# Optimization experiments

Hardware: AMD Instinct MI355X
Metric: run time of the kernel (lower is better)

The kernel has to match this reference:

```python
import jax, jax.numpy as jnp
import numpy as np

B, N, F, S, OUT = 8, 12000, 128, 16, 128

def setup_inputs() -> dict:
    key = jax.random.key(0)
    k1, k2, k3, k4 = jax.random.split(key, 4)
    x = jax.random.normal(k1, (B, N, F), dtype=jnp.float32)
    # Linear(in_c*spiral_size, out_c): weight [out, in], bias [out]
    bound = 1.0 / np.sqrt(F * S)
    W = jax.random.uniform(k2, (OUT, F * S), dtype=jnp.float32, minval=-bound, maxval=bound)
    b = jax.random.uniform(k3, (OUT,), dtype=jnp.float32, minval=-bound, maxval=bound)
    spiral_adj = jax.random.randint(k4, (1, N, S), 0, N, dtype=jnp.int32)
    zero_padding = jnp.ones((1, N, 1), dtype=jnp.float32)
    return {"x": x, "W": W, "b": b, "spiral_adj": spiral_adj, "zero_padding": zero_padding}

def reference(x, W, b, spiral_adj, zero_padding):
    # x: [B, N, F]; spiral_adj: [1, N, S] vertex indices shared across batch
    idx = spiral_adj[0]                         # [N, S]
    spirals = x[:, idx, :]                      # [B, N, S, F] gather along vertex dim
    bsz, npts, s, f = spirals.shape
    spirals = spirals.reshape(bsz, npts, s * f)  # [B, N, S*F]
    out = jnp.einsum('bnk,ok->bno', spirals, W) + b  # [B, N, OUT]
    out = jax.nn.relu(out)
    return out * zero_padding
```

## Files before the change

kernel.cpp:

```cpp
#include <hip/hip_runtime.h>

#define BATCH 8
#define NPTS  12000
#define FDIM  128
#define SDIM  16
#define ODIM  128
#define KDIM  (SDIM * FDIM)
#define MTOT  (BATCH * NPTS)

#define BM 128
#define BK 64

#define NTILES 94
#define XELEMS (BATCH * NPTS * FDIM)
#define WELEMS (ODIM * KDIM)
#define XBYTES ((size_t)XELEMS * 2)
#define WBYTES ((size_t)WELEMS * 2)

typedef __bf16 bf16x4 __attribute__((ext_vector_type(4)));
typedef __bf16 bf16x8 __attribute__((ext_vector_type(8)));
typedef float  f32x4  __attribute__((ext_vector_type(4)));
typedef float  f32x8  __attribute__((ext_vector_type(8)));

#define AS1(p) ((const __attribute__((address_space(1))) void*)(p))
#define AS3(p) ((__attribute__((address_space(3))) void*)(p))

#define CVT_XBLK 6000
#define CVT_WBLK 128
#define CVT_BPB  750

__global__ __launch_bounds__(256)
void cvt_f32_bf16(const float* __restrict__ x, const float* __restrict__ W,
                  __bf16* __restrict__ xb, __bf16* __restrict__ Wb) {
    const int blk = blockIdx.x;
    const float* __restrict__ src;
    __bf16* __restrict__ dst;
    size_t base;
    if (blk < CVT_XBLK) {
        const int b = blk & 7;
        const int c = blk >> 3;
        base = ((size_t)b * CVT_BPB + c) * (256 * 8) + (size_t)threadIdx.x * 8;
        src = x;  dst = xb;
    } else {
        base = (size_t)(blk - CVT_XBLK) * (256 * 8) + (size_t)threadIdx.x * 8;
        src = W;  dst = Wb;
    }
    const f32x8 v = *reinterpret_cast<const f32x8*>(src + base);
    bf16x8 h;
#pragma unroll
    for (int e = 0; e < 8; ++e) h[e] = (__bf16)v[e];
    *reinterpret_cast<bf16x8*>(dst + base) = h;
}

__global__ __launch_bounds__(256, 2)
void spiral_gemm_bf16(const __bf16* __restrict__ xb,
                      const __bf16* __restrict__ Wb,
                      const float*  __restrict__ bias,
                      const int*    __restrict__ idx,
                      const float*  __restrict__ zp,
                      float*        __restrict__ out)
{
    __shared__ __bf16 As[2][BM * BK];
    __shared__ __bf16 Ws[2][ODIM * BK];
    __shared__ int    idxS[BM * SDIM];

    const int tid   = threadIdx.x;
    const int wave  = tid >> 6;
    const int lane  = tid & 63;
    const int batch = blockIdx.x & 7;
    const int n0    = (blockIdx.x >> 3) * BM;

    const int lrow8 = lane >> 3;
    const int clog  = (lane & 7) ^ lrow8;

    const __bf16* xbase = xb + (size_t)batch * (NPTS * FDIM);

    {
        const int row  = tid >> 1, half = tid & 1;
        const int n    = n0 + row;
        const int nrow = n < NPTS ? n : NPTS - 1;
        const int4* s4 = reinterpret_cast<const int4*>(idx + nrow * SDIM + half * 8);
        int4* d4       = reinterpret_cast<int4*>(&idxS[row * SDIM + half * 8]);
        d4[0] = s4[0];
        d4[1] = s4[1];
    }
    __syncthreads();

    int rrow[4];
#pragma unroll
    for (int p = 0; p < 4; ++p) rrow[p] = (p * 4 + wave) * 8 + lrow8;

    int gCur[4], gNext[4];
#pragma unroll
    for (int p = 0; p < 4; ++p) gCur[p] = idxS[rrow[p] * SDIM + 0];

    auto issue = [&](int buf, int kt, const int* g) {
        const int f0 = (kt & 1) * BK;
#pragma unroll
        for (int p = 0; p < 4; ++p) {
            const int r0 = (p * 4 + wave) * 8;
            const __bf16* ga = xbase + (size_t)g[p] * FDIM + f0 + clog * 8;
            __builtin_amdgcn_global_load_lds(AS1(ga), AS3(&As[buf][r0 * BK]), 16, 0, 0);
            const __bf16* gw = Wb + (size_t)(r0 + lrow8) * KDIM + kt * BK + clog * 8;
            __builtin_amdgcn_global_load_lds(AS1(gw), AS3(&Ws[buf][r0 * BK]), 16, 0, 0);
        }
    };

    f32x4 acc[4][4];
#pragma unroll
    for (int i = 0; i < 4; ++i)
#pragma unroll
        for (int j = 0; j < 4; ++j)
            acc[i][j] = f32x4{0.f, 0.f, 0.f, 0.f};

    const int wm   = (wave >> 1) * 64;
    const int wn   = (wave & 1) * 64;
    const int lrow = lane & 15;
    const int quad = lane >> 4;

    auto compute = [&](int buf) {
#pragma unroll
        for (int kk = 0; kk < 2; ++kk) {
            const int ph = (kk * 4 + quad) ^ (lrow & 7);
            bf16x8 a[4], b[4];
#pragma unroll
            for (int i = 0; i < 4; ++i)
                a[i] = *reinterpret_cast<const bf16x8*>(
                    &As[buf][(wm + i * 16 + lrow) * BK + ph * 8]);
#pragma unroll
            for (int j = 0; j < 4; ++j)
                b[j] = *reinterpret_cast<const bf16x8*>(
                    &Ws[buf][(wn + j * 16 + lrow) * BK + ph * 8]);
#pragma unroll
            for (int i = 0; i < 4; ++i)
#pragma unroll
                for (int j = 0; j < 4; ++j)
                    acc[i][j] = __builtin_amdgcn_mfma_f32_16x16x32_bf16(
                        a[i], b[j], acc[i][j], 0, 0, 0);
        }
    };

    issue(0, 0, gCur);

    for (int t = 0; t < 16; ++t) {
        issue(1, 2 * t + 1, gCur);
        asm volatile("s_waitcnt vmcnt(8)" ::: "memory");
        asm volatile("s_barrier" ::: "memory");
        if (t < 15) {
#pragma unroll
            for (int p = 0; p < 4; ++p)
                gNext[p] = idxS[rrow[p] * SDIM + t + 1];
        }
        compute(0);
        asm volatile("s_barrier" ::: "memory");

        if (t < 15) {
            issue(0, 2 * t + 2, gNext);
            asm volatile("s_waitcnt vmcnt(8)" ::: "memory");
        } else {
            asm volatile("s_waitcnt vmcnt(0)" ::: "memory");
        }
        asm volatile("s_barrier" ::: "memory");
        compute(1);
        asm volatile("s_barrier" ::: "memory");
#pragma unroll
        for (int p = 0; p < 4; ++p) gCur[p] = gNext[p];
    }

#pragma unroll
    for (int i = 0; i < 4; ++i) {
#pragma unroll
        for (int r = 0; r < 4; ++r) {
            const int row = wm + i * 16 + quad * 4 + r;
            const int n   = n0 + row;
            if (n < NPTS) {
                const float z = zp[n];
                float* orow   = out + ((size_t)batch * NPTS + n) * ODIM;
#pragma unroll
                for (int j = 0; j < 4; ++j) {
                    const int col = wn + j * 16 + lrow;
                    float v = acc[i][j][r] + bias[col];
                    v = fmaxf(v, 0.f);
                    orow[col] = v * z;
                }
            }
        }
    }
}

#define LDA 72
__global__ __launch_bounds__(256, 2)
void spiral_gemm_fp32(const float* __restrict__ x, const float* __restrict__ W,
                      const float* __restrict__ bias, const int* __restrict__ idx,
                      const float* __restrict__ zp, float* __restrict__ out)
{
    __shared__ __bf16 Asf[BM * LDA];
    __shared__ __bf16 Wsf[ODIM * LDA];
    const int tid = threadIdx.x, wave = tid >> 6, lane = tid & 63;
    const int m0 = blockIdx.x * BM;
    const int srow = tid >> 3, schunk = tid & 7;
    int a_n[4]; const float* a_xb[4];
#pragma unroll
    for (int p = 0; p < 4; ++p) {
        int m = m0 + srow + p * 32, bb = m / NPTS;
        a_n[p] = m - bb * NPTS; a_xb[p] = x + (size_t)bb * (NPTS * FDIM);
    }
    f32x4 acc[4][4];
#pragma unroll
    for (int i = 0; i < 4; ++i)
#pragma unroll
        for (int j = 0; j < 4; ++j) acc[i][j] = f32x4{0.f,0.f,0.f,0.f};
    const int wm = (wave >> 1) * 64, wn = (wave & 1) * 64;
    const int lrow = lane & 15, quad = lane >> 4;
    for (int kt = 0; kt < KDIM / BK; ++kt) {
        const int s = kt >> 1, f0 = (kt & 1) * BK;
        __syncthreads();
#pragma unroll
        for (int p = 0; p < 4; ++p) {
            const int r = srow + p * 32;
            const int g = idx[a_n[p] * SDIM + s];
            const f32x8 v = *reinterpret_cast<const f32x8*>(
                a_xb[p] + (size_t)g * FDIM + f0 + schunk * 8);
            bf16x8 h;
#pragma unroll
            for (int e = 0; e < 8; ++e) h[e] = (__bf16)v[e];
            *reinterpret_cast<bf16x8*>(&Asf[r * LDA + schunk * 8]) = h;
            const f32x8 w = *reinterpret_cast<const f32x8*>(
                W + (size_t)r * KDIM + kt * BK + schunk * 8);
            bf16x8 hw;
#pragma unroll
            for (int e = 0; e < 8; ++e) hw[e] = (__bf16)w[e];
            *reinterpret_cast<bf16x8*>(&Wsf[r * LDA + schunk * 8]) = hw;
        }
        __syncthreads();
#pragma unroll
        for (int kk = 0; kk < 2; ++kk) {
            const int koff = kk * 32 + quad * 8;
            bf16x8 a[4], b[4];
#pragma unroll
            for (int i = 0; i < 4; ++i)
                a[i] = *reinterpret_cast<const bf16x8*>(&Asf[(wm + i*16 + lrow)*LDA + koff]);
#pragma unroll
            for (int j = 0; j < 4; ++j)
                b[j] = *reinterpret_cast<const bf16x8*>(&Wsf[(wn + j*16 + lrow)*LDA + koff]);
#pragma unroll
            for (int i = 0; i < 4; ++i)
#pragma unroll
                for (int j = 0; j < 4; ++j)
                    acc[i][j] = __builtin_amdgcn_mfma_f32_16x16x32_bf16(a[i], b[j], acc[i][j], 0,0,0);
        }
    }
#pragma unroll
    for (int i = 0; i < 4; ++i)
#pragma unroll
        for (int r = 0; r < 4; ++r) {
            const int row = wm + i * 16 + quad * 4 + r;
            const int m = m0 + row, bb = m / NPTS, nnn = m - bb * NPTS;
            const float z = zp[nnn];
            float* orow = out + (size_t)m * ODIM;
#pragma unroll
            for (int j = 0; j < 4; ++j) {
                const int col = wn + j * 16 + lrow;
                float v = acc[i][j][r] + bias[col];
                orow[col] = fmaxf(v, 0.f) * z;
            }
        }
}

extern "C" void kernel_launch(void* const* d_in, const int* in_sizes, int n_in,
                              void* d_out, int out_size, void* d_ws, size_t ws_size,
                              hipStream_t stream) {
    const float* x    = (const float*)d_in[0];
    const float* W    = (const float*)d_in[1];
    const float* bias = (const float*)d_in[2];
    const int*   idx  = (const int*)d_in[3];
    const float* zp   = (const float*)d_in[4];
    float*       out  = (float*)d_out;

    if (ws_size >= XBYTES + WBYTES) {
        __bf16* xb = (__bf16*)d_ws;
        __bf16* Wb = (__bf16*)((char*)d_ws + XBYTES);
        cvt_f32_bf16<<<dim3(CVT_XBLK + CVT_WBLK), dim3(256), 0, stream>>>(x, W, xb, Wb);
        spiral_gemm_bf16<<<dim3(BATCH * NTILES), dim3(256), 0, stream>>>(
            xb, Wb, bias, idx, zp, out);
    } else {
        spiral_gemm_fp32<<<dim3(MTOT / BM), dim3(256), 0, stream>>>(
            x, W, bias, idx, zp, out);
    }
}
```

Measured before the change: 163.4 us.

## Retile bf16 spiral GEMM to 192-row tiles with six waves and BK=32

Enlarges the M tile from 128 to 192 rows by running six waves per block, and halves the K step to 32, so each spiral slice now takes four pipeline stages instead of two. The gather loads, the XOR swizzle and the wait counts are rewritten to match, and only the first four waves load W. The goal is to reuse each W tile across more rows and cut block count (63 tiles per batch). The trade-off is twice as many barriers per K element, uneven load counts across waves, and a tile count that may fit the CU count less evenly.

```diff
diff --git a/kernel.cpp b/kernel.cpp
--- a/kernel.cpp
+++ b/kernel.cpp
@@ -8,10 +8,10 @@
 #define KDIM  (SDIM * FDIM)
 #define MTOT  (BATCH * NPTS)
 
-#define BM 128
-#define BK 64
-
-#define NTILES 94
+#define BM 192
+#define BK 32
+
+#define NTILES 63
 #define XELEMS (BATCH * NPTS * FDIM)
 #define WELEMS (ODIM * KDIM)
 #define XBYTES ((size_t)XELEMS * 2)
@@ -52,7 +52,7 @@
     *reinterpret_cast<bf16x8*>(dst + base) = h;
 }
 
-__global__ __launch_bounds__(256, 2)
+__global__ __launch_bounds__(384, 3)
 void spiral_gemm_bf16(const __bf16* __restrict__ xb,
                       const __bf16* __restrict__ Wb,
                       const float*  __restrict__ bias,
@@ -70,8 +70,8 @@
     const int batch = blockIdx.x & 7;
     const int n0    = (blockIdx.x >> 3) * BM;
 
-    const int lrow8 = lane >> 3;
-    const int clog  = (lane & 7) ^ lrow8;
+    const int lrow16 = lane >> 2;
+    const int clog   = (lane & 3) ^ ((lane >> 4) & 3);
 
     const __bf16* xbase = xb + (size_t)batch * (NPTS * FDIM);
 
@@ -86,24 +86,35 @@
     }
     __syncthreads();
 
-    int rrow[4];
-#pragma unroll
-    for (int p = 0; p < 4; ++p) rrow[p] = (p * 4 + wave) * 8 + lrow8;
-
-    int gCur[4], gNext[4];
-#pragma unroll
-    for (int p = 0; p < 4; ++p) gCur[p] = idxS[rrow[p] * SDIM + 0];
-
-    auto issue = [&](int buf, int kt, const int* g) {
-        const int f0 = (kt & 1) * BK;
-#pragma unroll
-        for (int p = 0; p < 4; ++p) {
-            const int r0 = (p * 4 + wave) * 8;
+    int rrow[2];
+#pragma unroll
+    for (int p = 0; p < 2; ++p) rrow[p] = wave * 32 + p * 16 + lrow16;
+
+    int gCur[2], gNext[2];
+#pragma unroll
+    for (int p = 0; p < 2; ++p) gCur[p] = idxS[rrow[p] * SDIM + 0];
+
+    auto issueA = [&](int buf, int f0, const int* g) {
+#pragma unroll
+        for (int p = 0; p < 2; ++p) {
+            const int r0 = wave * 32 + p * 16;
             const __bf16* ga = xbase + (size_t)g[p] * FDIM + f0 + clog * 8;
             __builtin_amdgcn_global_load_lds(AS1(ga), AS3(&As[buf][r0 * BK]), 16, 0, 0);
-            const __bf16* gw = Wb + (size_t)(r0 + lrow8) * KDIM + kt * BK + clog * 8;
-            __builtin_amdgcn_global_load_lds(AS1(gw), AS3(&Ws[buf][r0 * BK]), 16, 0, 0);
-        }
+        }
+    };
+    auto issueW = [&](int buf, int kt) {
+        if (wave < 4) {
+#pragma unroll
+            for (int p = 0; p < 2; ++p) {
+                const int r0 = wave * 32 + p * 16;
+                const __bf16* gw = Wb + (size_t)(r0 + lrow16) * KDIM + kt * BK + clog * 8;
+                __builtin_amdgcn_global_load_lds(AS1(gw), AS3(&Ws[buf][r0 * BK]), 16, 0, 0);
+            }
+        }
+    };
+    auto waitA = [&]() {
+        if (wave < 4) { asm volatile("s_waitcnt vmcnt(4)" ::: "memory"); }
+        else          { asm volatile("s_waitcnt vmcnt(2)" ::: "memory"); }
     };
 
     f32x4 acc[4][4];
@@ -117,46 +128,56 @@
     const int wn   = (wave & 1) * 64;
     const int lrow = lane & 15;
     const int quad = lane >> 4;
+    const int ph   = quad ^ ((lrow >> 2) & 3);
 
     auto compute = [&](int buf) {
-#pragma unroll
-        for (int kk = 0; kk < 2; ++kk) {
-            const int ph = (kk * 4 + quad) ^ (lrow & 7);
-            bf16x8 a[4], b[4];
-#pragma unroll
-            for (int i = 0; i < 4; ++i)
-                a[i] = *reinterpret_cast<const bf16x8*>(
-                    &As[buf][(wm + i * 16 + lrow) * BK + ph * 8]);
+        bf16x8 a[4], b[4];
+#pragma unroll
+        for (int i = 0; i < 4; ++i)
+            a[i] = *reinterpret_cast<const bf16x8*>(
+                &As[buf][(wm + i * 16 + lrow) * BK + ph * 8]);
+#pragma unroll
+        for (int j = 0; j < 4; ++j)
+            b[j] = *reinterpret_cast<const bf16x8*>(
+                &Ws[buf][(wn + j * 16 + lrow) * BK + ph * 8]);
+#pragma unroll
+        for (int i = 0; i < 4; ++i)
 #pragma unroll
             for (int j = 0; j < 4; ++j)
-                b[j] = *reinterpret_cast<const bf16x8*>(
-                    &Ws[buf][(wn + j * 16 + lrow) * BK + ph * 8]);
-#pragma unroll
-            for (int i = 0; i < 4; ++i)
-#pragma unroll
-                for (int j = 0; j < 4; ++j)
-                    acc[i][j] = __builtin_amdgcn_mfma_f32_16x16x32_bf16(
-                        a[i], b[j], acc[i][j], 0, 0, 0);
-        }
+                acc[i][j] = __builtin_amdgcn_mfma_f32_16x16x32_bf16(
+                    a[i], b[j], acc[i][j], 0, 0, 0);
     };
 
-    issue(0, 0, gCur);
+    issueA(0, 0, gCur);
+    issueW(0, 0);
 
     for (int t = 0; t < 16; ++t) {
-        issue(1, 2 * t + 1, gCur);
-        asm volatile("s_waitcnt vmcnt(8)" ::: "memory");
+        issueA(1, 32, gCur);  issueW(1, 4 * t + 1);
+        waitA();
         asm volatile("s_barrier" ::: "memory");
         if (t < 15) {
 #pragma unroll
-            for (int p = 0; p < 4; ++p)
+            for (int p = 0; p < 2; ++p)
                 gNext[p] = idxS[rrow[p] * SDIM + t + 1];
         }
         compute(0);
         asm volatile("s_barrier" ::: "memory");
 
+        issueA(0, 64, gCur);  issueW(0, 4 * t + 2);
+        waitA();
+        asm volatile("s_barrier" ::: "memory");
+        compute(1);
+        asm volatile("s_barrier" ::: "memory");
+
+        issueA(1, 96, gCur);  issueW(1, 4 * t + 3);
+        waitA();
+        asm volatile("s_barrier" ::: "memory");
+        compute(0);
+        asm volatile("s_barrier" ::: "memory");
+
         if (t < 15) {
-            issue(0, 2 * t + 2, gNext);
-            asm volatile("s_waitcnt vmcnt(8)" ::: "memory");
+            issueA(0, 0, gNext);  issueW(0, 4 * t + 4);
+            waitA();
         } else {
             asm volatile("s_waitcnt vmcnt(0)" ::: "memory");
         }
@@ -164,7 +185,7 @@
         compute(1);
         asm volatile("s_barrier" ::: "memory");
 #pragma unroll
-        for (int p = 0; p < 4; ++p) gCur[p] = gNext[p];
+        for (int p = 0; p < 2; ++p) gCur[p] = gNext[p];
     }
 
 #pragma unroll
@@ -189,15 +210,16 @@
 }
 
 #define LDA 72
+#define BMF 128
 __global__ __launch_bounds__(256, 2)
 void spiral_gemm_fp32(const float* __restrict__ x, const float* __restrict__ W,
                       const float* __restrict__ bias, const int* __restrict__ idx,
                       const float* __restrict__ zp, float* __restrict__ out)
 {
-    __shared__ __bf16 Asf[BM * LDA];
+    __shared__ __bf16 Asf[BMF * LDA];
     __shared__ __bf16 Wsf[ODIM * LDA];
     const int tid = threadIdx.x, wave = tid >> 6, lane = tid & 63;
-    const int m0 = blockIdx.x * BM;
+    const int m0 = blockIdx.x * BMF;
     const int srow = tid >> 3, schunk = tid & 7;
     int a_n[4]; const float* a_xb[4];
 #pragma unroll
@@ -212,8 +234,8 @@
         for (int j = 0; j < 4; ++j) acc[i][j] = f32x4{0.f,0.f,0.f,0.f};
     const int wm = (wave >> 1) * 64, wn = (wave & 1) * 64;
     const int lrow = lane & 15, quad = lane >> 4;
-    for (int kt = 0; kt < KDIM / BK; ++kt) {
-        const int s = kt >> 1, f0 = (kt & 1) * BK;
+    for (int kt = 0; kt < KDIM / 64; ++kt) {
+        const int s = kt >> 1, f0 = (kt & 1) * 64;
         __syncthreads();
 #pragma unroll
         for (int p = 0; p < 4; ++p) {
@@ -226,7 +248,7 @@
             for (int e = 0; e < 8; ++e) h[e] = (__bf16)v[e];
             *reinterpret_cast<bf16x8*>(&Asf[r * LDA + schunk * 8]) = h;
             const f32x8 w = *reinterpret_cast<const f32x8*>(
-                W + (size_t)r * KDIM + kt * BK + schunk * 8);
+                W + (size_t)r * KDIM + kt * 64 + schunk * 8);
             bf16x8 hw;
 #pragma unroll
             for (int e = 0; e < 8; ++e) hw[e] = (__bf16)w[e];
@@ -281,10 +303,10 @@
         __bf16* xb = (__bf16*)d_ws;
         __bf16* Wb = (__bf16*)((char*)d_ws + XBYTES);
         cvt_f32_bf16<<<dim3(CVT_XBLK + CVT_WBLK), dim3(256), 0, stream>>>(x, W, xb, Wb);
-        spiral_gemm_bf16<<<dim3(BATCH * NTILES), dim3(256), 0, stream>>>(
+        spiral_gemm_bf16<<<dim3(BATCH * NTILES), dim3(384), 0, stream>>>(
             xb, Wb, bias, idx, zp, out);
     } else {
-        spiral_gemm_fp32<<<dim3(MTOT / BM), dim3(256), 0, stream>>>(
+        spiral_gemm_fp32<<<dim3(MTOT / BMF), dim3(256), 0, stream>>>(
             x, W, bias, idx, zp, out);
     }
 }
```

Measured after the change: 187.2 us. +14.6%, slower.
